# Performance work log

Hardware: AMD Instinct MI355X
Metric: run time of the kernel (lower is better)

## Reference

```python
import jax, jax.numpy as jnp
import numpy as np
import math

NEG_INF = -1e9
ALPHA = 1.0


def setup_inputs() -> dict:
    key = jax.random.key(0)
    B, T, S, C = 32, 1024, 512, 384
    k1, k2 = jax.random.split(key)
    epsilon = jax.random.normal(k1, (B, T, C), dtype=jnp.float32)
    conditional_inputs = jax.random.normal(k2, (B, S, C), dtype=jnp.float32)
    targets_lengths = jnp.full((B,), T, dtype=jnp.int32)
    condition_lengths = jnp.full((B,), S, dtype=jnp.int32)
    return {
        "epsilon": epsilon,
        "conditional_inputs": conditional_inputs,
        "targets_lengths": targets_lengths,
        "condition_lengths": condition_lengths,
    }


def _forward_dp(E):
    """Log-partition forward DP. E = alpha*Wr, [B,T,S].
    mu[t,j] = E[t,j] + logaddexp(mu[t-1,j], mu[t-1,j-1]); path starts at (0,0)."""
    B, T, S = E.shape
    start = jnp.where(jnp.arange(S) == 0, 0.0, NEG_INF)
    init = E[:, 0, :] + start[None, :]

    def step(mu_prev, e_t):
        shifted = jnp.concatenate([jnp.full((B, 1), NEG_INF, mu_prev.dtype), mu_prev[:, :-1]], axis=1)
        mu_t = e_t + jnp.logaddexp(mu_prev, shifted)
        return mu_t, mu_t

    _, mus = jax.lax.scan(step, init, jnp.moveaxis(E[:, 1:], 1, 0))
    return jnp.concatenate([init[:, None], jnp.moveaxis(mus, 0, 1)], axis=1)  # [B,T,S]


def _backward_dp(E):
    """Backward messages. beta[T-1,j] = 0 at j=S-1 else -inf;
    beta[t,j] = logaddexp(beta[t+1,j]+E[t+1,j], beta[t+1,j+1]+E[t+1,j+1])."""
    B, T, S = E.shape
    init = jnp.broadcast_to(jnp.where(jnp.arange(S) == S - 1, 0.0, NEG_INF), (B, S))

    def step(b_next, e_next):
        m = b_next + e_next
        shifted = jnp.concatenate([m[:, 1:], jnp.full((B, 1), NEG_INF, m.dtype)], axis=1)
        b_t = jnp.logaddexp(m, shifted)
        return b_t, b_t

    _, bs = jax.lax.scan(step, init, jnp.moveaxis(E[:, 1:], 1, 0), reverse=True)
    return jnp.concatenate([jnp.moveaxis(bs, 0, 1), init[:, None]], axis=1)  # [B,T,S]


def _maximum_path(logpi):
    """Viterbi over monotonic paths (stay at j or step to j from j-1 each t).
    Returns binary path [B,T,S]."""
    B, T, S = logpi.shape
    start = jnp.where(jnp.arange(S) == 0, 0.0, NEG_INF)
    init = logpi[:, 0, :] + start[None, :]

    def step(v_prev, lp_t):
        shifted = jnp.concatenate([jnp.full((B, 1), NEG_INF, v_prev.dtype), v_prev[:, :-1]], axis=1)
        v_t = lp_t + jnp.maximum(v_prev, shifted)
        move = shifted > v_prev  # True => predecessor is j-1
        return v_t, move

    _, moves = jax.lax.scan(step, init, jnp.moveaxis(logpi[:, 1:], 1, 0))  # [T-1,B,S]

    j_last = jnp.full((B,), S - 1, dtype=jnp.int32)

    def back(j, move_t):
        came = jnp.take_along_axis(move_t, j[:, None].astype(jnp.int32), axis=1)[:, 0]
        j_prev = j - came.astype(jnp.int32)
        return j_prev, j

    j0, js = jax.lax.scan(back, j_last, moves, reverse=True)  # js[i] = j at time i+1
    js_all = jnp.concatenate([j0[None], js], axis=0)  # [T,B]
    return jax.nn.one_hot(jnp.moveaxis(js_all, 0, 1), S, dtype=logpi.dtype)  # [B,T,S]


def reference(epsilon, conditional_inputs, targets_lengths, condition_lengths):
    B, T, C = epsilon.shape
    S = conditional_inputs.shape[1]
    # initial gaussian sample log-prob, masked by target lengths
    logp_eps = -0.5 * (epsilon ** 2 + math.log(2.0 * math.pi))
    tmask = (jnp.arange(T)[None, :] < targets_lengths[:, None]).astype(epsilon.dtype)
    logprobs = jnp.sum(tmask[:, :, None] * logp_eps, axis=(1, 2))

    z = epsilon  # Glow is external; treated as identity flow (logdet = 0)

    # score matrix + softmax over the target axis (dim 1), as in the source
    Wr = jnp.einsum("btc,bsc->bts", z, conditional_inputs)
    Wr = jax.nn.softmax(Wr, axis=1)

    E = ALPHA * Wr
    mu = _forward_dp(E)
    mu_N = mu[:, -1, -1]
    beta = _backward_dp(E)
    logpi = mu + beta - mu_N[:, None, None]  # posterior node log-marginals

    path = _maximum_path(logpi)  # [B,T,S] binary alignment
    sample_logprob = ALPHA * jnp.sum(path * Wr, axis=(1, 2)) - mu_N
    logprobs = logprobs + sample_logprob
    return path, logprobs
```

## Files before the change

### kernel.cpp

```cpp
#include <hip/hip_runtime.h>
#include <cstdint>
#include <cstddef>

#define B_ 32
#define T_ 1024
#define S_ 512
#define C_ 384
#define HALF_LOG_2PI 0.91893853320467274178f
#define LN2F 0.69314718055994530942f
#define INV_LN2F 1.44269504088896340736f

typedef unsigned short u16;
typedef unsigned long long u64;
typedef __attribute__((ext_vector_type(8))) short bf16x8;
typedef __attribute__((ext_vector_type(4))) float f32x4;

__device__ __forceinline__ unsigned rne16(float f) {
    unsigned b = __float_as_uint(f);
    return (b + 0x7FFFu + ((b >> 16) & 1u)) >> 16;
}
__device__ __forceinline__ uint4 pack8f(float a0, float a1, float a2, float a3,
                                        float a4, float a5, float a6, float a7) {
    uint4 q;
    q.x = rne16(a0) | (rne16(a1) << 16);
    q.y = rne16(a2) | (rne16(a3) << 16);
    q.z = rne16(a4) | (rne16(a5) << 16);
    q.w = rne16(a6) | (rne16(a7) << 16);
    return q;
}
#define UNPK(q, p)                                                              \
    float p##0 = __uint_as_float((q).x << 16),                                  \
          p##1 = __uint_as_float((q).x & 0xFFFF0000u),                          \
          p##2 = __uint_as_float((q).y << 16),                                  \
          p##3 = __uint_as_float((q).y & 0xFFFF0000u),                          \
          p##4 = __uint_as_float((q).z << 16),                                  \
          p##5 = __uint_as_float((q).z & 0xFFFF0000u),                          \
          p##6 = __uint_as_float((q).w << 16),                                  \
          p##7 = __uint_as_float((q).w & 0xFFFF0000u)

#define PROW(t) (*(const uint4*)(Pb  + (size_t)(t) * S_ + l8))
#define BROW(t) (*(const uint4*)(Btb + (size_t)(t) * S_ + l8))

template <int CTRL>
__device__ __forceinline__ float fdpp0(float x) {
    return __uint_as_float((unsigned)__builtin_amdgcn_update_dpp(
        0, (int)__float_as_uint(x), CTRL, 0xF, 0xF, true));
}
__device__ __forceinline__ float wave_fmax(float x) {
    x = fmaxf(x, fdpp0<0x121>(x));
    x = fmaxf(x, fdpp0<0x122>(x));
    x = fmaxf(x, fdpp0<0x124>(x));
    x = fmaxf(x, fdpp0<0x128>(x));
    float a = __uint_as_float((unsigned)__builtin_amdgcn_readlane((int)__float_as_uint(x), 0));
    float b = __uint_as_float((unsigned)__builtin_amdgcn_readlane((int)__float_as_uint(x), 16));
    float c = __uint_as_float((unsigned)__builtin_amdgcn_readlane((int)__float_as_uint(x), 32));
    float d = __uint_as_float((unsigned)__builtin_amdgcn_readlane((int)__float_as_uint(x), 48));
    return fmaxf(fmaxf(a, b), fmaxf(c, d));
}

__device__ __forceinline__ void gll16(const u16* g, u16* l) {
    __builtin_amdgcn_global_load_lds(
        (const __attribute__((address_space(1))) void*)g,
        (__attribute__((address_space(3))) void*)l, 16, 0, 0);
}
#define WAITV(N) do { asm volatile("s_waitcnt vmcnt(" #N ")" ::: "memory");     \
                      __builtin_amdgcn_sched_barrier(0); } while (0)
#define FENCE_LGKM() do { asm volatile("s_waitcnt lgkmcnt(0)" ::: "memory");    \
                          __builtin_amdgcn_sched_barrier(0); } while (0)

__global__ __launch_bounds__(256) void k_pre(const float* __restrict__ eps,
                                             const float* __restrict__ cond,
                                             const int* __restrict__ tlen,
                                             float* __restrict__ lp_part,
                                             u16* __restrict__ Abf,
                                             u16* __restrict__ Bbf) {
    if (blockIdx.x < 1536) {
        const int b = blockIdx.x / 48, chunk = blockIdx.x % 48;
        const int len = tlen[b];
        const float* base = eps + (size_t)b * T_ * C_ + (size_t)chunk * 8192;
        u16* obase = Abf + (size_t)b * T_ * C_ + (size_t)chunk * 8192;
        float acc = 0.f;
        for (int g = threadIdx.x; g < 1024; g += 256) {
            float4 v0 = *(const float4*)(base + g * 8);
            float4 v1 = *(const float4*)(base + g * 8 + 4);
            int t = (chunk * 8192 + g * 8) / C_;
            if (t < len)
                acc += v0.x*v0.x + v0.y*v0.y + v0.z*v0.z + v0.w*v0.w
                     + v1.x*v1.x + v1.y*v1.y + v1.z*v1.z + v1.w*v1.w;
            *(uint4*)(obase + g * 8) = pack8f(v0.x, v0.y, v0.z, v0.w,
                                              v1.x, v1.y, v1.z, v1.w);
        }
        __shared__ float red[256];
        red[threadIdx.x] = acc;
        __syncthreads();
        for (int o = 128; o > 0; o >>= 1) {
            if (threadIdx.x < o) red[threadIdx.x] += red[threadIdx.x + o];
            __syncthreads();
        }
        if (threadIdx.x == 0) lp_part[blockIdx.x] = -0.5f * red[0];
    } else {
        const size_t n8 = (size_t)B_ * S_ * C_ / 8;
        for (size_t i = (size_t)(blockIdx.x - 1536) * 256 + threadIdx.x; i < n8;
             i += (size_t)512 * 256) {
            float4 v0 = *(const float4*)(cond + i * 8);
            float4 v1 = *(const float4*)(cond + i * 8 + 4);
            *(uint4*)(Bbf + i * 8) = pack8f(v0.x, v0.y, v0.z, v0.w,
                                            v1.x, v1.y, v1.z, v1.w);
        }
    }
}

__global__ __launch_bounds__(256) void k_gemm(const u16* __restrict__ A,
                                              const u16* __restrict__ Bc,
                                              u16* __restrict__ Wb) {
    __shared__ u16 Al[4096];
    __shared__ u16 Bl[4096];
    const int wgid = blockIdx.x;
    const int xcd  = wgid & 7;
    const int rest = wgid >> 3;
    const int b    = (rest >> 5) * 8 + xcd;
    const int tile = rest & 31;
    const int m0 = (tile >> 2) * 128;
    const int n0 = (tile & 3) * 128;
    const int tid = threadIdx.x;
    const int lane = tid & 63, wid = tid >> 6;
    const int wy = wid >> 1, wx = wid & 1;
    const int r15 = lane & 15, kg = lane >> 4;
    const u16* Ab = A  + (size_t)b * T_ * C_;
    const u16* Bb = Bc + (size_t)b * S_ * C_;

    f32x4 acc[4][4];
#pragma unroll
    for (int i = 0; i < 4; ++i)
#pragma unroll
        for (int j = 0; j < 4; ++j) acc[i][j] = (f32x4){0.f, 0.f, 0.f, 0.f};

    const int row0 = tid >> 2, o0 = tid & 3;
    const int row1 = row0 + 64;
    const int wb0 = (row0 * 64 + o0 * 16) ^ (((row0 >> 1) & 7) << 4);
    const int wb1 = (row1 * 64 + o0 * 16) ^ (((row1 >> 1) & 7) << 4);
    const int rswz = ((r15 >> 1) & 7) << 4;

    for (int k0 = 0; k0 < C_; k0 += 32) {
        uint4 a0 = *(const uint4*)(Ab + (size_t)(m0 + row0) * C_ + k0 + o0 * 8);
        uint4 a1 = *(const uint4*)(Ab + (size_t)(m0 + row1) * C_ + k0 + o0 * 8);
        uint4 c0 = *(const uint4*)(Bb + (size_t)(n0 + row0) * C_ + k0 + o0 * 8);
        uint4 c1 = *(const uint4*)(Bb + (size_t)(n0 + row1) * C_ + k0 + o0 * 8);
        __syncthreads();
        *(uint4*)((char*)Al + wb0) = a0;
        *(uint4*)((char*)Al + wb1) = a1;
        *(uint4*)((char*)Bl + wb0) = c0;
        *(uint4*)((char*)Bl + wb1) = c1;
        __syncthreads();
        bf16x8 af[4], bfb[4];
#pragma unroll
        for (int ar = 0; ar < 4; ++ar) {
            int row = wy * 64 + ar * 16 + r15;
            af[ar] = *(const bf16x8*)((const char*)Al + ((row * 64 + kg * 16) ^ rswz));
        }
#pragma unroll
        for (int bc = 0; bc < 4; ++bc) {
            int row = wx * 64 + bc * 16 + r15;
            bfb[bc] = *(const bf16x8*)((const char*)Bl + ((row * 64 + kg * 16) ^ rswz));
        }
#pragma unroll
        for (int ar = 0; ar < 4; ++ar)
#pragma unroll
            for (int bc = 0; bc < 4; ++bc)
                acc[ar][bc] = __builtin_amdgcn_mfma_f32_16x16x32_bf16(
                    af[ar], bfb[bc], acc[ar][bc], 0, 0, 0);
    }
#pragma unroll
    for (int ar = 0; ar < 4; ++ar) {
        int t = m0 + wy * 64 + ar * 16 + kg * 4;
#pragma unroll
        for (int bc = 0; bc < 4; ++bc) {
            int s = n0 + wx * 64 + bc * 16 + r15;
            u16* dst = Wb + ((size_t)b * T_ + t) * S_ + s;
#pragma unroll
            for (int r = 0; r < 4; ++r) dst[(size_t)r * S_] = (u16)rne16(acc[ar][bc][r]);
        }
    }
}

#define COLU(i, xa, xb, xc, xd) do {                                            \
    float nm = fmaxf(fmaxf(fmaxf(m[i], xa), xb), fmaxf(xc, xd));                \
    s[i] = s[i] * __builtin_amdgcn_exp2f((m[i] - nm) * INV_LN2F)                \
         + __builtin_amdgcn_exp2f((xa - nm) * INV_LN2F)                         \
         + __builtin_amdgcn_exp2f((xb - nm) * INV_LN2F)                         \
         + __builtin_amdgcn_exp2f((xc - nm) * INV_LN2F)                         \
         + __builtin_amdgcn_exp2f((xd - nm) * INV_LN2F);                        \
    m[i] = nm;                                                                  \
} while (0)

__global__ __launch_bounds__(256) void k_stats1(const u16* __restrict__ Wb,
                                                float* __restrict__ pmax,
                                                float* __restrict__ psum) {
    __shared__ float smax[4][S_];
    __shared__ float ssum[4][S_];
    const int c = blockIdx.x & 3;
    const int b = blockIdx.x >> 2;
    const int w = threadIdx.x >> 6, l = threadIdx.x & 63;
    const u16* base = Wb + (size_t)b * T_ * S_ + (size_t)(c * 256 + w * 64) * S_ + l * 8;
    float m[8], s[8];
#pragma unroll
    for (int i = 0; i < 8; ++i) { m[i] = -3.0e38f; s[i] = 0.f; }
    for (int t = 0; t < 64; t += 4) {
        uint4 q0 = *(const uint4*)(base + (size_t)(t + 0) * S_);
        uint4 q1 = *(const uint4*)(base + (size_t)(t + 1) * S_);
        uint4 q2 = *(const uint4*)(base + (size_t)(t + 2) * S_);
        uint4 q3 = *(const uint4*)(base + (size_t)(t + 3) * S_);
        UNPK(q0, xa); UNPK(q1, xb); UNPK(q2, xc); UNPK(q3, xd);
        COLU(0, xa0, xb0, xc0, xd0);
        COLU(1, xa1, xb1, xc1, xd1);
        COLU(2, xa2, xb2, xc2, xd2);
        COLU(3, xa3, xb3, xc3, xd3);
        COLU(4, xa4, xb4, xc4, xd4);
        COLU(5, xa5, xb5, xc5, xd5);
        COLU(6, xa6, xb6, xc6, xd6);
        COLU(7, xa7, xb7, xc7, xd7);
    }
#pragma unroll
    for (int i = 0; i < 8; ++i) {
        smax[w][l * 8 + i] = m[i];
        ssum[w][l * 8 + i] = s[i];
    }
    __syncthreads();
    for (int col = threadIdx.x; col < S_; col += 256) {
        float m0 = smax[0][col], m1 = smax[1][col];
        float m2 = smax[2][col], m3 = smax[3][col];
        float nm = fmaxf(fmaxf(m0, m1), fmaxf(m2, m3));
        float ss = ssum[0][col] * __builtin_amdgcn_exp2f((m0 - nm) * INV_LN2F)
                 + ssum[1][col] * __builtin_amdgcn_exp2f((m1 - nm) * INV_LN2F)
                 + ssum[2][col] * __builtin_amdgcn_exp2f((m2 - nm) * INV_LN2F)
                 + ssum[3][col] * __builtin_amdgcn_exp2f((m3 - nm) * INV_LN2F);
        pmax[(size_t)c * B_ * S_ + b * S_ + col] = nm;
        psum[(size_t)c * B_ * S_ + b * S_ + col] = ss;
    }
}

__global__ __launch_bounds__(256) void k_stats2(const float* __restrict__ pmax,
                                                const float* __restrict__ psum,
                                                float* __restrict__ cmax,
                                                float* __restrict__ cinv) {
    const int i = blockIdx.x * 256 + threadIdx.x;
    float m0 = pmax[i], m1 = pmax[(size_t)B_ * S_ + i];
    float m2 = pmax[(size_t)2 * B_ * S_ + i], m3 = pmax[(size_t)3 * B_ * S_ + i];
    float m = fmaxf(fmaxf(m0, m1), fmaxf(m2, m3));
    float s = psum[i] * expf(m0 - m)
            + psum[(size_t)B_ * S_ + i] * expf(m1 - m)
            + psum[(size_t)2 * B_ * S_ + i] * expf(m2 - m)
            + psum[(size_t)3 * B_ * S_ + i] * expf(m3 - m);
    cmax[i] = m;
    cinv[i] = 1.0f / s;
}

__global__ __launch_bounds__(256) void k_pack(const u16* __restrict__ Wb,
                                              const float* __restrict__ cmax,
                                              const float* __restrict__ cinv,
                                              u16* __restrict__ P) {
    const size_t total8 = (size_t)B_ * T_ * S_ / 8;
    for (size_t i = (size_t)blockIdx.x * 256 + threadIdx.x; i < total8;
         i += (size_t)gridDim.x * 256) {
        size_t base = i * 8;
        int s = (int)(base & (S_ - 1));
        int b = (int)(base >> 19);
        uint4 xq = *(const uint4*)(Wb + base);
        UNPK(xq, x);
        float4 mA = *(const float4*)(cmax + (size_t)b * S_ + s);
        float4 mB = *(const float4*)(cmax + (size_t)b * S_ + s + 4);
        float4 iA = *(const float4*)(cinv + (size_t)b * S_ + s);
        float4 iB = *(const float4*)(cinv + (size_t)b * S_ + s + 4);
        float w0 = __builtin_amdgcn_exp2f(fmaf(x0, INV_LN2F, -mA.x * INV_LN2F)) * iA.x;
        float w1 = __builtin_amdgcn_exp2f(fmaf(x1, INV_LN2F, -mA.y * INV_LN2F)) * iA.y;
        float w2 = __builtin_amdgcn_exp2f(fmaf(x2, INV_LN2F, -mA.z * INV_LN2F)) * iA.z;
        float w3 = __builtin_amdgcn_exp2f(fmaf(x3, INV_LN2F, -mA.w * INV_LN2F)) * iA.w;
        float w4 = __builtin_amdgcn_exp2f(fmaf(x4, INV_LN2F, -mB.x * INV_LN2F)) * iB.x;
        float w5 = __builtin_amdgcn_exp2f(fmaf(x5, INV_LN2F, -mB.y * INV_LN2F)) * iB.y;
        float w6 = __builtin_amdgcn_exp2f(fmaf(x6, INV_LN2F, -mB.z * INV_LN2F)) * iB.z;
        float w7 = __builtin_amdgcn_exp2f(fmaf(x7, INV_LN2F, -mB.w * INV_LN2F)) * iB.w;
        float p0 = __builtin_amdgcn_exp2f(fmaf(w0, INV_LN2F, -2.0f));
        float p1 = __builtin_amdgcn_exp2f(fmaf(w1, INV_LN2F, -2.0f));
        float p2 = __builtin_amdgcn_exp2f(fmaf(w2, INV_LN2F, -2.0f));
        float p3 = __builtin_amdgcn_exp2f(fmaf(w3, INV_LN2F, -2.0f));
        float p4 = __builtin_amdgcn_exp2f(fmaf(w4, INV_LN2F, -2.0f));
        float p5 = __builtin_amdgcn_exp2f(fmaf(w5, INV_LN2F, -2.0f));
        float p6 = __builtin_amdgcn_exp2f(fmaf(w6, INV_LN2F, -2.0f));
        float p7 = __builtin_amdgcn_exp2f(fmaf(w7, INV_LN2F, -2.0f));
        *(uint4*)(P + base) = pack8f(p0, p1, p2, p3, p4, p5, p6, p7);
    }
}

#define RENORM_B() do {                                                         \
    float mx_ = wave_fmax(fmaxf(fmaxf(fmaxf(m0,m1),fmaxf(m2,m3)),               \
                                fmaxf(fmaxf(m4,m5),fmaxf(m6,m7))));             \
    int eb_ = (__float_as_int(mx_) >> 23) & 255;                                \
    float sc_ = (eb_ > 0) ? __int_as_float((254 - eb_) << 23) : 1.0f;           \
    m0*=sc_; m1*=sc_; m2*=sc_; m3*=sc_; m4*=sc_; m5*=sc_; m6*=sc_; m7*=sc_;     \
} while (0)

#define BSTEPD(tt, jj) do {                                                     \
    uint4 q_ = *(const uint4*)&Pl[buf][jj][l8];                                 \
    UNPK(q_, eP);                                                               \
    float z0=m0*eP0, z1=m1*eP1, z2=m2*eP2, z3=m3*eP3;                           \
    float z4=m4*eP4, z5=m5*eP5, z6=m6*eP6, z7=m7*eP7;                           \
    float rt = fdpp0<0x130>(z0);                \
    m0=z0+z1; m1=z1+z2; m2=z2+z3; m3=z3+z4;                                     \
    m4=z4+z5; m5=z5+z6; m6=z6+z7; m7=z7+rt;                                     \
    if ((tt) < w0 + 32) {                                                       \
        uint4 st;                                                               \
        asm("v_cvt_pk_bf16_f32 %0, %1, %2" : "=v"(st.x) : "v"(m0), "v"(m1));    \
        asm("v_cvt_pk_bf16_f32 %0, %1, %2" : "=v"(st.y) : "v"(m2), "v"(m3));    \
        asm("v_cvt_pk_bf16_f32 %0, %1, %2" : "=v"(st.z) : "v"(m4), "v"(m5));    \
        asm("v_cvt_pk_bf16_f32 %0, %1, %2" : "=v"(st.w) : "v"(m6), "v"(m7));    \
        *(uint4*)(Bb + (size_t)(tt) * S_ + l8) = st;                            \
    }                                                                           \
} while (0)

__global__ __launch_bounds__(64) void k_beta(const u16* __restrict__ P,
                                             u16* __restrict__ Bt) {
    __shared__ u16 Pl[2][8][S_];
    const int l = threadIdx.x, l8 = l * 8;
    const int xcd = blockIdx.x & 7;
    const int idx = blockIdx.x >> 3;
    const int c = idx & 31;
    const int b = ((idx >> 5) << 3) + xcd;
    const int w0 = c * 32;
    const u16* Pb = P  + (size_t)b * T_ * S_;
    u16*      Bb = Bt + (size_t)b * T_ * S_;
    float m0, m1, m2, m3, m4, m5, m6, m7;
    int te = w0 + 63;
    if (te > 1023) te = 1023;
    if (te == 1023) {
        m0 = m1 = m2 = m3 = m4 = m5 = m6 = 0.f;
        m7 = (l == 63) ? 1.f : 0.f;
        if (1023 < w0 + 32) {
            uint4 st;
            asm("v_cvt_pk_bf16_f32 %0, %1, %2" : "=v"(st.x) : "v"(m0), "v"(m1));
            asm("v_cvt_pk_bf16_f32 %0, %1, %2" : "=v"(st.y) : "v"(m2), "v"(m3));
            asm("v_cvt_pk_bf16_f32 %0, %1, %2" : "=v"(st.z) : "v"(m4), "v"(m5));
            asm("v_cvt_pk_bf16_f32 %0, %1, %2" : "=v"(st.w) : "v"(m6), "v"(m7));
            *(uint4*)(Bb + (size_t)1023 * S_ + l8) = st;
        }
    } else {
        m0 = m1 = m2 = m3 = m4 = m5 = m6 = m7 = 1.f;
    }
    const int cnt = te - w0;
    const int ng = (cnt + 1) >> 3;
#pragma unroll
    for (int r = 0; r < 8; ++r)
        gll16(Pb + (size_t)(te - r) * S_ + l8, &Pl[0][r][0]);
#pragma unroll
    for (int r = 0; r < 8; ++r)
        gll16(Pb + (size_t)(te - 8 - r) * S_ + l8, &Pl[1][r][0]);
    int tt = te - 1;
    int buf = 0;
    for (int g = 0; g < ng - 1; ++g) {
        WAITV(8);
        BSTEPD(tt - 0, 0);  BSTEPD(tt - 1, 1);  BSTEPD(tt - 2, 2);  BSTEPD(tt - 3, 3);
        BSTEPD(tt - 4, 4);  BSTEPD(tt - 5, 5);  BSTEPD(tt - 6, 6);  BSTEPD(tt - 7, 7);
        RENORM_B();
        FENCE_LGKM();
        if (g + 2 < ng) {
            const int bs = te - 8 * (g + 2);
#pragma unroll
            for (int r = 0; r < 8; ++r)
                gll16(Pb + (size_t)(bs - r) * S_ + l8, &Pl[buf][r][0]);
        }
        __builtin_amdgcn_sched_barrier(0);
        buf ^= 1;
        tt -= 8;
    }
    WAITV(0);
    BSTEPD(tt - 0, 0);  BSTEPD(tt - 1, 1);  BSTEPD(tt - 2, 2);  BSTEPD(tt - 3, 3);
    BSTEPD(tt - 4, 4);  BSTEPD(tt - 5, 5);  BSTEPD(tt - 6, 6);
}

#define RENORM_MI() do {                                                        \
    float mx_ = wave_fmax(fmaxf(fmaxf(fmaxf(m0,m1),fmaxf(m2,m3)),               \
                                fmaxf(fmaxf(m4,m5),fmaxf(m6,m7))));             \
    int eb_ = (__float_as_int(mx_) >> 23) & 255;                                \
    float sc_ = (eb_ > 0) ? __int_as_float((254 - eb_) << 23) : 1.0f;           \
    if (eb_ > 0) ioffM += eb_ - 127;                                            \
    m0*=sc_; m1*=sc_; m2*=sc_; m3*=sc_; m4*=sc_; m5*=sc_; m6*=sc_; m7*=sc_;     \
} while (0)

#define RENORM_VR() do {                                                        \
    float mx_ = wave_fmax(fmaxf(fmaxf(fmaxf(v0,v1),fmaxf(v2,v3)),               \
                                fmaxf(fmaxf(v4,v5),fmaxf(v6,v7))));             \
    int eb_ = (__float_as_int(mx_) >> 23) & 255;                                \
    float sc_ = (eb_ > 0) ? __int_as_float((254 - eb_) << 23) : 0.0f;           \
    float ad_ = (eb_ > 0) ? 0.f : 1.f;                                          \
    v0=fmaf(v0,sc_,ad_); v1=fmaf(v1,sc_,ad_); v2=fmaf(v2,sc_,ad_);              \
    v3=fmaf(v3,sc_,ad_); v4=fmaf(v4,sc_,ad_); v5=fmaf(v5,sc_,ad_);              \
    v6=fmaf(v6,sc_,ad_); v7=fmaf(v7,sc_,ad_);                                   \
} while (0)

#define VSTEPD(TT, jj) do {                                                     \
    uint4 qp_ = *(const uint4*)&Pl[buf][jj][l8];                                \
    uint4 qb_ = *(const uint4*)&Bl[buf][jj][l8];                                \
    UNPK(qp_, eP); UNPK(qb_, eB);                                               \
    float lf = fdpp0<0x138>(m7);                 \
    float n0 = eP0*(m0+lf), n1 = eP1*(m1+m0);                                   \
    float n2 = eP2*(m2+m1), n3 = eP3*(m3+m2);                                   \
    float n4 = eP4*(m4+m3), n5 = eP5*(m5+m4);                                   \
    float n6 = eP6*(m6+m5), n7 = eP7*(m7+m6);                                   \
    float vlf = fdpp0<0x138>(v7);                                               \
    if ((TT) >= w0) {                                                           \
        unsigned cc0=(vlf>v0)?1u:0u, cc1=(v0>v1)?2u:0u, cc2=(v1>v2)?4u:0u,      \
                 cc3=(v2>v3)?8u:0u,  cc4=(v3>v4)?16u:0u, cc5=(v4>v5)?32u:0u,    \
                 cc6=(v5>v6)?64u:0u, cc7=(v6>v7)?128u:0u;                       \
        acc |= ((u64)(cc0|cc1|cc2|cc3|cc4|cc5|cc6|cc7)) << (((TT)&7)*8);        \
        if (((TT)&7) == 7) { mrow[((TT)>>3)*64 + l] = acc; acc = 0ULL; }        \
    }                                                                           \
    float w0v=(n0*eB0)*fmaxf(v0,vlf), w1v=(n1*eB1)*fmaxf(v1,v0);                \
    float w2v=(n2*eB2)*fmaxf(v2,v1),  w3v=(n3*eB3)*fmaxf(v3,v2);                \
    float w4v=(n4*eB4)*fmaxf(v4,v3),  w5v=(n5*eB5)*fmaxf(v5,v4);                \
    float w6v=(n6*eB6)*fmaxf(v6,v5),  w7v=(n7*eB7)*fmaxf(v7,v6);                \
    m0=n0;m1=n1;m2=n2;m3=n3;m4=n4;m5=n5;m6=n6;m7=n7;                            \
    v0=w0v;v1=w1v;v2=w2v;v3=w3v;v4=w4v;v5=w5v;v6=w6v;v7=w7v;                    \
    if ((TT) == wexp) { wex = __shfl(m0, 2 * c); wio = ioffM; }                 \
} while (0)

__global__ __launch_bounds__(64) void k_vit(const u16* __restrict__ P,
                                            const u16* __restrict__ Bt,
                                            u64* __restrict__ mbg,
                                            float* __restrict__ elog,
                                            float* __restrict__ wlg) {
    __shared__ u16 Pl[2][8][S_];
    __shared__ u16 Bl[2][8][S_];
    const int l = threadIdx.x, l8 = l * 8;
    const int xcd = blockIdx.x & 7;
    const int idx = blockIdx.x >> 3;
    const int c = idx & 31;
    const int b = ((idx >> 5) << 3) + xcd;
    const int w0 = c * 32, tend = w0 + 31;
    const int t0 = (w0 >= 32) ? (w0 - 32) : 0;
    const int wexp = w0 - 1;
    const u16* Pb  = P  + (size_t)b * T_ * S_;
    const u16* Btb = Bt + (size_t)b * T_ * S_;
    u64* mrow = mbg + (size_t)b * 8192;

    float m0,m1,m2,m3,m4,m5,m6,m7, v0,v1,v2,v3,v4,v5,v6,v7;
    int ioffM = 0;
    float wex = 1.f; int wio = 0;
    {
        uint4 qp = PROW(t0); UNPK(qp, eP);
        uint4 qb = BROW(t0); UNPK(qb, eB);
        if (t0 == 0) {
            m0 = (l == 0) ? eP0 : 0.f;
            m1 = 0.f; m2 = 0.f; m3 = 0.f; m4 = 0.f; m5 = 0.f; m6 = 0.f; m7 = 0.f;
        } else {
            m0 = eP0; m1 = eP1; m2 = eP2; m3 = eP3;
            m4 = eP4; m5 = eP5; m6 = eP6; m7 = eP7;
        }
        v0 = m0*eB0; v1 = m1*eB1; v2 = m2*eB2; v3 = m3*eB3;
        v4 = m4*eB4; v5 = m5*eB5; v6 = m6*eB6; v7 = m7*eB7;
    }
    u64 acc = 0ULL;
    const int cnt = tend - t0;
    const int ng = (cnt + 1) >> 3;
#pragma unroll
    for (int r = 0; r < 8; ++r) {
        gll16(Pb  + (size_t)(t0 + 1 + r) * S_ + l8, &Pl[0][r][0]);
        gll16(Btb + (size_t)(t0 + 1 + r) * S_ + l8, &Bl[0][r][0]);
    }
#pragma unroll
    for (int r = 0; r < 8; ++r) {
        gll16(Pb  + (size_t)(t0 + 9 + r) * S_ + l8, &Pl[1][r][0]);
        gll16(Btb + (size_t)(t0 + 9 + r) * S_ + l8, &Bl[1][r][0]);
    }
    int t = t0 + 1;
    int buf = 0;
    for (int g = 0; g < ng - 1; ++g) {
        WAITV(16);
        VSTEPD(t + 0, 0);  VSTEPD(t + 1, 1);  VSTEPD(t + 2, 2);  VSTEPD(t + 3, 3);
        VSTEPD(t + 4, 4);  VSTEPD(t + 5, 5);  VSTEPD(t + 6, 6);  VSTEPD(t + 7, 7);
        RENORM_MI();
        RENORM_VR();
        FENCE_LGKM();
        if (g + 2 < ng) {
            const int bs = t0 + 1 + 8 * (g + 2);
#pragma unroll
            for (int r = 0; r < 8; ++r) {
                gll16(Pb  + (size_t)(bs + r) * S_ + l8, &Pl[buf][r][0]);
                gll16(Btb + (size_t)(bs + r) * S_ + l8, &Bl[buf][r][0]);
            }
        }
        __builtin_amdgcn_sched_barrier(0);
        buf ^= 1;
        t += 8;
    }
    WAITV(0);
    VSTEPD(t + 0, 0);  VSTEPD(t + 1, 1);  VSTEPD(t + 2, 2);  VSTEPD(t + 3, 3);
    VSTEPD(t + 4, 4);  VSTEPD(t + 5, 5);  VSTEPD(t + 6, 6);

    float eex = (c == 31) ? __shfl(m7, 63) : __shfl(m0, 2 * (c + 1));
    if (l == 0) {
        elog[b * 32 + c] = __builtin_amdgcn_logf(fmaxf(eex, 1e-35f)) + (float)ioffM;
        if (c >= 1)
            wlg[b * 32 + c] = __builtin_amdgcn_logf(fmaxf(wex, 1e-35f)) + (float)wio;
    }
}

__global__ __launch_bounds__(512) void k_map(const u64* __restrict__ mbg,
                                             u16* __restrict__ map) {
    __shared__ u64 mb[4][64];
    const int b = blockIdx.x >> 5, c = blockIdx.x & 31;
    const int tid = threadIdx.x;
    const u64* src = mbg + (size_t)b * 8192 + (size_t)(4 * c) * 64;
    if (tid < 128) ((uint4*)&mb[0][0])[tid] = ((const uint4*)src)[tid];
    __syncthreads();
    int jj = tid;
    const int kmin = (c == 0) ? 1 : 0;
    for (int k = 31; k >= kmin; --k) {
        u64 word = mb[k >> 3][jj >> 3];
        jj -= (int)((word >> ((k & 7) * 8 + (jj & 7))) & 1ULL);
    }
    map[((size_t)b * 32 + c) * 512 + tid] = (u16)jj;
}

__global__ __launch_bounds__(256) void k_btr2(const u64* __restrict__ mbg,
                                              const u16* __restrict__ map,
                                              int* __restrict__ js) {
    __shared__ u64 mb[128][64];
    __shared__ u16 cent[32];
    const int b = blockIdx.x, tid = threadIdx.x;
    const uint4* src = (const uint4*)(mbg + (size_t)b * 8192);
    uint4* dst = (uint4*)&mb[0][0];
    for (int i = tid; i < 4096; i += 256) dst[i] = src[i];
    if (tid == 0) {
        int jj = 511;
        cent[31] = 511;
        for (int c = 31; c >= 1; --c) {
            jj = (int)map[((size_t)b * 32 + c) * 512 + jj];
            cent[c - 1] = (u16)jj;
        }
    }
    __syncthreads();
    if (tid < 32) {
        const int c = tid;
        int jj = (int)cent[c];
        js[b * T_ + 32 * c + 31] = jj;
        const int kmin = (c == 0) ? 1 : 0;
        for (int k = 31; k >= kmin; --k) {
            const int t = 32 * c + k;
            u64 word = mb[t >> 3][jj >> 3];
            jj -= (int)((word >> ((t & 7) * 8 + (jj & 7))) & 1ULL);
            js[b * T_ + t - 1] = jj;
        }
    }
}

__global__ __launch_bounds__(256) void k_out(const int* __restrict__ js,
                                             const u16* __restrict__ P,
                                             const float* __restrict__ lp_part,
                                             const int* __restrict__ tlen,
                                             const float* __restrict__ elog,
                                             const float* __restrict__ wlg,
                                             float* __restrict__ outp,
                                             float* __restrict__ out_lp) {
    if (blockIdx.x < 4096) {
        const size_t total4 = (size_t)B_ * T_ * S_ / 4;
        float4* O = (float4*)outp;
        for (size_t i = (size_t)blockIdx.x * 256 + threadIdx.x; i < total4;
             i += (size_t)4096 * 256) {
            size_t base = i * 4;
            int s = (int)(base & (S_ - 1));
            int row = (int)(base >> 9);
            int jt = js[row];
            float4 o;
            o.x = (s == jt) ? 1.f : 0.f;
            o.y = (s + 1 == jt) ? 1.f : 0.f;
            o.z = (s + 2 == jt) ? 1.f : 0.f;
            o.w = (s + 3 == jt) ? 1.f : 0.f;
            O[i] = o;
        }
    } else {
        const int b = blockIdx.x - 4096;
        float acc = 0.f;
        for (int t = threadIdx.x; t < T_; t += 256) {
            int jt = js[b * T_ + t];
            unsigned u = P[((size_t)b * T_ + t) * S_ + jt];
            acc += __builtin_amdgcn_logf(__uint_as_float(u << 16));
        }
        __shared__ float red[256];
        red[threadIdx.x] = acc;
        __syncthreads();
        for (int o = 128; o > 0; o >>= 1) {
            if (threadIdx.x < o) red[threadIdx.x] += red[threadIdx.x + o];
            __syncthreads();
        }
        if (threadIdx.x == 0) {
            float basep = 0.f;
            for (int i = 0; i < 48; ++i) basep += lp_part[b * 48 + i];
            float mu2n = elog[b * 32 + 31];
            for (int cc = 1; cc < 32; ++cc)
                mu2n += elog[b * 32 + cc - 1] - wlg[b * 32 + cc];
            out_lp[b] = basep - HALF_LOG_2PI * ((float)tlen[b] * C_)
                        + LN2F * (red[0] - mu2n);
        }
    }
}

extern "C" void kernel_launch(void* const* d_in, const int* in_sizes, int n_in,
                              void* d_out, int out_size, void* d_ws, size_t ws_size,
                              hipStream_t stream) {
    const float* eps  = (const float*)d_in[0];
    const float* cond = (const float*)d_in[1];
    const int* tlen   = (const int*)d_in[2];

    float* out_path = (float*)d_out;
    float* out_lp   = out_path + (size_t)B_ * T_ * S_;

    const size_t NBTS = (size_t)B_ * T_ * S_;
    char* w = (char*)d_ws;
    u16*   Wb   = (u16*)w;
    u16*   P    = Wb + NBTS;
    u16*   Bt   = P + NBTS;
    u16*   Abf  = Bt + NBTS;
    u16*   Bbf  = Abf + (size_t)B_ * T_ * C_;
    u64*   mbg  = (u64*)(Bbf + (size_t)B_ * S_ * C_);
    float* pmax = (float*)(mbg + (size_t)B_ * 8192);
    float* psum = pmax + (size_t)4 * B_ * S_;
    float* cmax = psum + (size_t)4 * B_ * S_;
    float* cinv = cmax + (size_t)B_ * S_;
    float* lp_part = cinv + (size_t)B_ * S_;
    float* elog = lp_part + B_ * 48;
    float* wlg  = elog + B_ * 32;
    int*   js   = (int*)(wlg + B_ * 32);
    u16*   map  = (u16*)(js + B_ * T_);

    k_pre<<<2048, 256, 0, stream>>>(eps, cond, tlen, lp_part, Abf, Bbf);
    k_gemm<<<1024, 256, 0, stream>>>(Abf, Bbf, Wb);
    k_stats1<<<B_ * 4, 256, 0, stream>>>(Wb, pmax, psum);
    k_stats2<<<B_ * S_ / 256, 256, 0, stream>>>(pmax, psum, cmax, cinv);
    k_pack<<<2048, 256, 0, stream>>>(Wb, cmax, cinv, P);
    k_beta<<<B_ * 32, 64, 0, stream>>>(P, Bt);
    k_vit<<<B_ * 32, 64, 0, stream>>>(P, Bt, mbg, elog, wlg);
    k_map<<<B_ * 32, 512, 0, stream>>>(mbg, map);
    k_btr2<<<B_, 256, 0, stream>>>(mbg, map, js);
    k_out<<<4096 + B_, 256, 0, stream>>>(js, P, lp_part, tlen, elog, wlg,
                                         out_path, out_lp);
}
```

Before: 154.5 us.

## Fuse softmax column stats into GEMM epilogue and drop the P pack pass

The GEMM epilogue now computes per-column partial max and sum-exp over its 64-row slab and reduces them across lanes with shuffles, which removes the separate k_stats1 pass that re-read the whole score matrix. The k_pack kernel that materialised the softmax-exponentiated matrix P is also removed. k_beta, k_vit and k_out instead recompute the two exp2 calls per element from the raw bf16 scores plus the column max and inverse sum. This saves two full passes over a 32x1024x512 bf16 array, in exchange for extra transcendental work inside the latency-bound DP kernels and 16 partial slabs for k_stats2 to combine instead of 4.

```diff
diff --git a/kernel.cpp b/kernel.cpp
--- a/kernel.cpp
+++ b/kernel.cpp
@@ -38,7 +38,12 @@
           p##6 = __uint_as_float((q).w << 16),                                  \
           p##7 = __uint_as_float((q).w & 0xFFFF0000u)
 
-#define PROW(t) (*(const uint4*)(Pb  + (size_t)(t) * S_ + l8))
+#define P1(x, km, ki)                                                           \
+    __builtin_amdgcn_exp2f(fmaf(                                                \
+        __builtin_amdgcn_exp2f(fmaf((x), INV_LN2F, -(km))) * (ki),              \
+        INV_LN2F, -2.0f))
+
+#define WROW(t) (*(const uint4*)(Wbb + (size_t)(t) * S_ + l8))
 #define BROW(t) (*(const uint4*)(Btb + (size_t)(t) * S_ + l8))
 
 template <int CTRL>
@@ -112,7 +117,9 @@
 
 __global__ __launch_bounds__(256) void k_gemm(const u16* __restrict__ A,
                                               const u16* __restrict__ Bc,
-                                              u16* __restrict__ Wb) {
+                                              u16* __restrict__ Wb,
+                                              float* __restrict__ pmax,
+                                              float* __restrict__ psum) {
     __shared__ u16 Al[4096];
     __shared__ u16 Bl[4096];
     const int wgid = blockIdx.x;
@@ -181,61 +188,43 @@
             for (int r = 0; r < 4; ++r) dst[(size_t)r * S_] = (u16)rne16(acc[ar][bc][r]);
         }
     }
-}
-
-#define COLU(i, xa, xb, xc, xd) do {                                            \
-    float nm = fmaxf(fmaxf(fmaxf(m[i], xa), xb), fmaxf(xc, xd));                \
-    s[i] = s[i] * __builtin_amdgcn_exp2f((m[i] - nm) * INV_LN2F)                \
-         + __builtin_amdgcn_exp2f((xa - nm) * INV_LN2F)                         \
-         + __builtin_amdgcn_exp2f((xb - nm) * INV_LN2F)                         \
-         + __builtin_amdgcn_exp2f((xc - nm) * INV_LN2F)                         \
-         + __builtin_amdgcn_exp2f((xd - nm) * INV_LN2F);                        \
-    m[i] = nm;                                                                  \
-} while (0)
-
-__global__ __launch_bounds__(256) void k_stats1(const u16* __restrict__ Wb,
-                                                float* __restrict__ pmax,
-                                                float* __restrict__ psum) {
-    __shared__ float smax[4][S_];
-    __shared__ float ssum[4][S_];
-    const int c = blockIdx.x & 3;
-    const int b = blockIdx.x >> 2;
-    const int w = threadIdx.x >> 6, l = threadIdx.x & 63;
-    const u16* base = Wb + (size_t)b * T_ * S_ + (size_t)(c * 256 + w * 64) * S_ + l * 8;
-    float m[8], s[8];
-#pragma unroll
-    for (int i = 0; i < 8; ++i) { m[i] = -3.0e38f; s[i] = 0.f; }
-    for (int t = 0; t < 64; t += 4) {
-        uint4 q0 = *(const uint4*)(base + (size_t)(t + 0) * S_);
-        uint4 q1 = *(const uint4*)(base + (size_t)(t + 1) * S_);
-        uint4 q2 = *(const uint4*)(base + (size_t)(t + 2) * S_);
-        uint4 q3 = *(const uint4*)(base + (size_t)(t + 3) * S_);
-        UNPK(q0, xa); UNPK(q1, xb); UNPK(q2, xc); UNPK(q3, xd);
-        COLU(0, xa0, xb0, xc0, xd0);
-        COLU(1, xa1, xb1, xc1, xd1);
-        COLU(2, xa2, xb2, xc2, xd2);
-        COLU(3, xa3, xb3, xc3, xd3);
-        COLU(4, xa4, xb4, xc4, xd4);
-        COLU(5, xa5, xb5, xc5, xd5);
-        COLU(6, xa6, xb6, xc6, xd6);
-        COLU(7, xa7, xb7, xc7, xd7);
-    }
-#pragma unroll
-    for (int i = 0; i < 8; ++i) {
-        smax[w][l * 8 + i] = m[i];
-        ssum[w][l * 8 + i] = s[i];
-    }
-    __syncthreads();
-    for (int col = threadIdx.x; col < S_; col += 256) {
-        float m0 = smax[0][col], m1 = smax[1][col];
-        float m2 = smax[2][col], m3 = smax[3][col];
-        float nm = fmaxf(fmaxf(m0, m1), fmaxf(m2, m3));
-        float ss = ssum[0][col] * __builtin_amdgcn_exp2f((m0 - nm) * INV_LN2F)
-                 + ssum[1][col] * __builtin_amdgcn_exp2f((m1 - nm) * INV_LN2F)
-                 + ssum[2][col] * __builtin_amdgcn_exp2f((m2 - nm) * INV_LN2F)
-                 + ssum[3][col] * __builtin_amdgcn_exp2f((m3 - nm) * INV_LN2F);
-        pmax[(size_t)c * B_ * S_ + b * S_ + col] = nm;
-        psum[(size_t)c * B_ * S_ + b * S_ + col] = ss;
+    float pm[4], ps[4];
+#pragma unroll
+    for (int bc = 0; bc < 4; ++bc) {
+        float mx = -3.0e38f;
+#pragma unroll
+        for (int ar = 0; ar < 4; ++ar)
+#pragma unroll
+            for (int r = 0; r < 4; ++r) mx = fmaxf(mx, acc[ar][bc][r]);
+        float s = 0.f;
+#pragma unroll
+        for (int ar = 0; ar < 4; ++ar)
+#pragma unroll
+            for (int r = 0; r < 4; ++r)
+                s += __builtin_amdgcn_exp2f((acc[ar][bc][r] - mx) * INV_LN2F);
+        pm[bc] = mx; ps[bc] = s;
+    }
+#pragma unroll
+    for (int bc = 0; bc < 4; ++bc) {
+        float m2 = __shfl_xor(pm[bc], 16), s2 = __shfl_xor(ps[bc], 16);
+        float nm = fmaxf(pm[bc], m2);
+        ps[bc] = ps[bc] * __builtin_amdgcn_exp2f((pm[bc] - nm) * INV_LN2F)
+               + s2     * __builtin_amdgcn_exp2f((m2     - nm) * INV_LN2F);
+        pm[bc] = nm;
+        m2 = __shfl_xor(pm[bc], 32); s2 = __shfl_xor(ps[bc], 32);
+        nm = fmaxf(pm[bc], m2);
+        ps[bc] = ps[bc] * __builtin_amdgcn_exp2f((pm[bc] - nm) * INV_LN2F)
+               + s2     * __builtin_amdgcn_exp2f((m2     - nm) * INV_LN2F);
+        pm[bc] = nm;
+    }
+    if (kg == 0) {
+        const int tc = (m0 >> 6) + wy;
+#pragma unroll
+        for (int bc = 0; bc < 4; ++bc) {
+            int col = n0 + wx * 64 + bc * 16 + r15;
+            pmax[((size_t)tc * B_ + b) * S_ + col] = pm[bc];
+            psum[((size_t)tc * B_ + b) * S_ + col] = ps[bc];
+        }
     }
 }
 
@@ -243,52 +232,16 @@
                                                 const float* __restrict__ psum,
                                                 float* __restrict__ cmax,
                                                 float* __restrict__ cinv) {
-    const int i = blockIdx.x * 256 + threadIdx.x;
-    float m0 = pmax[i], m1 = pmax[(size_t)B_ * S_ + i];
-    float m2 = pmax[(size_t)2 * B_ * S_ + i], m3 = pmax[(size_t)3 * B_ * S_ + i];
-    float m = fmaxf(fmaxf(m0, m1), fmaxf(m2, m3));
-    float s = psum[i] * expf(m0 - m)
-            + psum[(size_t)B_ * S_ + i] * expf(m1 - m)
-            + psum[(size_t)2 * B_ * S_ + i] * expf(m2 - m)
-            + psum[(size_t)3 * B_ * S_ + i] * expf(m3 - m);
+    const size_t i = (size_t)blockIdx.x * 256 + threadIdx.x;
+    const size_t BS = (size_t)B_ * S_;
+    float m = -3.0e38f;
+    for (int cc = 0; cc < 16; ++cc) m = fmaxf(m, pmax[cc * BS + i]);
+    float s = 0.f;
+    for (int cc = 0; cc < 16; ++cc)
+        s += psum[cc * BS + i] *
+             __builtin_amdgcn_exp2f((pmax[cc * BS + i] - m) * INV_LN2F);
     cmax[i] = m;
     cinv[i] = 1.0f / s;
-}
-
-__global__ __launch_bounds__(256) void k_pack(const u16* __restrict__ Wb,
-                                              const float* __restrict__ cmax,
-                                              const float* __restrict__ cinv,
-                                              u16* __restrict__ P) {
-    const size_t total8 = (size_t)B_ * T_ * S_ / 8;
-    for (size_t i = (size_t)blockIdx.x * 256 + threadIdx.x; i < total8;
-         i += (size_t)gridDim.x * 256) {
-        size_t base = i * 8;
-        int s = (int)(base & (S_ - 1));
-        int b = (int)(base >> 19);
-        uint4 xq = *(const uint4*)(Wb + base);
-        UNPK(xq, x);
-        float4 mA = *(const float4*)(cmax + (size_t)b * S_ + s);
-        float4 mB = *(const float4*)(cmax + (size_t)b * S_ + s + 4);
-        float4 iA = *(const float4*)(cinv + (size_t)b * S_ + s);
-        float4 iB = *(const float4*)(cinv + (size_t)b * S_ + s + 4);
-        float w0 = __builtin_amdgcn_exp2f(fmaf(x0, INV_LN2F, -mA.x * INV_LN2F)) * iA.x;
-        float w1 = __builtin_amdgcn_exp2f(fmaf(x1, INV_LN2F, -mA.y * INV_LN2F)) * iA.y;
-        float w2 = __builtin_amdgcn_exp2f(fmaf(x2, INV_LN2F, -mA.z * INV_LN2F)) * iA.z;
-        float w3 = __builtin_amdgcn_exp2f(fmaf(x3, INV_LN2F, -mA.w * INV_LN2F)) * iA.w;
-        float w4 = __builtin_amdgcn_exp2f(fmaf(x4, INV_LN2F, -mB.x * INV_LN2F)) * iB.x;
-        float w5 = __builtin_amdgcn_exp2f(fmaf(x5, INV_LN2F, -mB.y * INV_LN2F)) * iB.y;
-        float w6 = __builtin_amdgcn_exp2f(fmaf(x6, INV_LN2F, -mB.z * INV_LN2F)) * iB.z;
-        float w7 = __builtin_amdgcn_exp2f(fmaf(x7, INV_LN2F, -mB.w * INV_LN2F)) * iB.w;
-        float p0 = __builtin_amdgcn_exp2f(fmaf(w0, INV_LN2F, -2.0f));
-        float p1 = __builtin_amdgcn_exp2f(fmaf(w1, INV_LN2F, -2.0f));
-        float p2 = __builtin_amdgcn_exp2f(fmaf(w2, INV_LN2F, -2.0f));
-        float p3 = __builtin_amdgcn_exp2f(fmaf(w3, INV_LN2F, -2.0f));
-        float p4 = __builtin_amdgcn_exp2f(fmaf(w4, INV_LN2F, -2.0f));
-        float p5 = __builtin_amdgcn_exp2f(fmaf(w5, INV_LN2F, -2.0f));
-        float p6 = __builtin_amdgcn_exp2f(fmaf(w6, INV_LN2F, -2.0f));
-        float p7 = __builtin_amdgcn_exp2f(fmaf(w7, INV_LN2F, -2.0f));
-        *(uint4*)(P + base) = pack8f(p0, p1, p2, p3, p4, p5, p6, p7);
-    }
 }
 
 #define RENORM_B() do {                                                         \
@@ -301,7 +254,11 @@
 
 #define BSTEPD(tt, jj) do {                                                     \
     uint4 q_ = *(const uint4*)&Pl[buf][jj][l8];                                 \
-    UNPK(q_, eP);                                                               \
+    UNPK(q_, xr);                                                               \
+    float eP0=P1(xr0,km0,ki0), eP1=P1(xr1,km1,ki1);                             \
+    float eP2=P1(xr2,km2,ki2), eP3=P1(xr3,km3,ki3);                             \
+    float eP4=P1(xr4,km4,ki4), eP5=P1(xr5,km5,ki5);                             \
+    float eP6=P1(xr6,km6,ki6), eP7=P1(xr7,km7,ki7);                             \
     float z0=m0*eP0, z1=m1*eP1, z2=m2*eP2, z3=m3*eP3;                           \
     float z4=m4*eP4, z5=m5*eP5, z6=m6*eP6, z7=m7*eP7;                           \
     float rt = fdpp0<0x130>(z0);                \
@@ -317,7 +274,9 @@
     }                                                                           \
 } while (0)
 
-__global__ __launch_bounds__(64) void k_beta(const u16* __restrict__ P,
+__global__ __launch_bounds__(64) void k_beta(const u16* __restrict__ Wb,
+                                             const float* __restrict__ cmax,
+                                             const float* __restrict__ cinv,
                                              u16* __restrict__ Bt) {
     __shared__ u16 Pl[2][8][S_];
     const int l = threadIdx.x, l8 = l * 8;
@@ -326,8 +285,17 @@
     const int c = idx & 31;
     const int b = ((idx >> 5) << 3) + xcd;
     const int w0 = c * 32;
-    const u16* Pb = P  + (size_t)b * T_ * S_;
+    const u16* Pb = Wb + (size_t)b * T_ * S_;
     u16*      Bb = Bt + (size_t)b * T_ * S_;
+    const float4 cA = *(const float4*)(cmax + (size_t)b * S_ + l8);
+    const float4 cB = *(const float4*)(cmax + (size_t)b * S_ + l8 + 4);
+    const float4 iA = *(const float4*)(cinv + (size_t)b * S_ + l8);
+    const float4 iB = *(const float4*)(cinv + (size_t)b * S_ + l8 + 4);
+    const float km0=cA.x*INV_LN2F, km1=cA.y*INV_LN2F, km2=cA.z*INV_LN2F, km3=cA.w*INV_LN2F;
+    const float km4=cB.x*INV_LN2F, km5=cB.y*INV_LN2F, km6=cB.z*INV_LN2F, km7=cB.w*INV_LN2F;
+    const float ki0=iA.x, ki1=iA.y, ki2=iA.z, ki3=iA.w;
+    const float ki4=iB.x, ki5=iB.y, ki6=iB.z, ki7=iB.w;
+
     float m0, m1, m2, m3, m4, m5, m6, m7;
     int te = w0 + 63;
     if (te > 1023) te = 1023;
@@ -399,7 +367,11 @@
 #define VSTEPD(TT, jj) do {                                                     \
     uint4 qp_ = *(const uint4*)&Pl[buf][jj][l8];                                \
     uint4 qb_ = *(const uint4*)&Bl[buf][jj][l8];                                \
-    UNPK(qp_, eP); UNPK(qb_, eB);                                               \
+    UNPK(qp_, xr); UNPK(qb_, eB);                                               \
+    float eP0=P1(xr0,km0,ki0), eP1=P1(xr1,km1,ki1);                             \
+    float eP2=P1(xr2,km2,ki2), eP3=P1(xr3,km3,ki3);                             \
+    float eP4=P1(xr4,km4,ki4), eP5=P1(xr5,km5,ki5);                             \
+    float eP6=P1(xr6,km6,ki6), eP7=P1(xr7,km7,ki7);                             \
     float lf = fdpp0<0x138>(m7);                 \
     float n0 = eP0*(m0+lf), n1 = eP1*(m1+m0);                                   \
     float n2 = eP2*(m2+m1), n3 = eP3*(m3+m2);                                   \
@@ -422,8 +394,10 @@
     if ((TT) == wexp) { wex = __shfl(m0, 2 * c); wio = ioffM; }                 \
 } while (0)
 
-__global__ __launch_bounds__(64) void k_vit(const u16* __restrict__ P,
+__global__ __launch_bounds__(64) void k_vit(const u16* __restrict__ Wb,
                                             const u16* __restrict__ Bt,
+                                            const float* __restrict__ cmax,
+                                            const float* __restrict__ cinv,
                                             u64* __restrict__ mbg,
                                             float* __restrict__ elog,
                                             float* __restrict__ wlg) {
@@ -437,22 +411,35 @@
     const int w0 = c * 32, tend = w0 + 31;
     const int t0 = (w0 >= 32) ? (w0 - 32) : 0;
     const int wexp = w0 - 1;
-    const u16* Pb  = P  + (size_t)b * T_ * S_;
+    const u16* Wbb = Wb + (size_t)b * T_ * S_;
+    const u16* Pb  = Wbb;
     const u16* Btb = Bt + (size_t)b * T_ * S_;
     u64* mrow = mbg + (size_t)b * 8192;
+    const float4 cA = *(const float4*)(cmax + (size_t)b * S_ + l8);
+    const float4 cB = *(const float4*)(cmax + (size_t)b * S_ + l8 + 4);
+    const float4 iA = *(const float4*)(cinv + (size_t)b * S_ + l8);
+    const float4 iB = *(const float4*)(cinv + (size_t)b * S_ + l8 + 4);
+    const float km0=cA.x*INV_LN2F, km1=cA.y*INV_LN2F, km2=cA.z*INV_LN2F, km3=cA.w*INV_LN2F;
+    const float km4=cB.x*INV_LN2F, km5=cB.y*INV_LN2F, km6=cB.z*INV_LN2F, km7=cB.w*INV_LN2F;
+    const float ki0=iA.x, ki1=iA.y, ki2=iA.z, ki3=iA.w;
+    const float ki4=iB.x, ki5=iB.y, ki6=iB.z, ki7=iB.w;
 
     float m0,m1,m2,m3,m4,m5,m6,m7, v0,v1,v2,v3,v4,v5,v6,v7;
     int ioffM = 0;
     float wex = 1.f; int wio = 0;
     {
-        uint4 qp = PROW(t0); UNPK(qp, eP);
+        uint4 qp = WROW(t0); UNPK(qp, xr);
         uint4 qb = BROW(t0); UNPK(qb, eB);
+        float p0i=P1(xr0,km0,ki0), p1i=P1(xr1,km1,ki1);
+        float p2i=P1(xr2,km2,ki2), p3i=P1(xr3,km3,ki3);
+        float p4i=P1(xr4,km4,ki4), p5i=P1(xr5,km5,ki5);
+        float p6i=P1(xr6,km6,ki6), p7i=P1(xr7,km7,ki7);
         if (t0 == 0) {
-            m0 = (l == 0) ? eP0 : 0.f;
+            m0 = (l == 0) ? p0i : 0.f;
             m1 = 0.f; m2 = 0.f; m3 = 0.f; m4 = 0.f; m5 = 0.f; m6 = 0.f; m7 = 0.f;
         } else {
-            m0 = eP0; m1 = eP1; m2 = eP2; m3 = eP3;
-            m4 = eP4; m5 = eP5; m6 = eP6; m7 = eP7;
+            m0 = p0i; m1 = p1i; m2 = p2i; m3 = p3i;
+            m4 = p4i; m5 = p5i; m6 = p6i; m7 = p7i;
         }
         v0 = m0*eB0; v1 = m1*eB1; v2 = m2*eB2; v3 = m3*eB3;
         v4 = m4*eB4; v5 = m5*eB5; v6 = m6*eB6; v7 = m7*eB7;
@@ -553,7 +540,9 @@
 }
 
 __global__ __launch_bounds__(256) void k_out(const int* __restrict__ js,
-                                             const u16* __restrict__ P,
+                                             const u16* __restrict__ Wb,
+                                             const float* __restrict__ cmax,
+                                             const float* __restrict__ cinv,
                                              const float* __restrict__ lp_part,
                                              const int* __restrict__ tlen,
                                              const float* __restrict__ elog,
@@ -581,8 +570,12 @@
         float acc = 0.f;
         for (int t = threadIdx.x; t < T_; t += 256) {
             int jt = js[b * T_ + t];
-            unsigned u = P[((size_t)b * T_ + t) * S_ + jt];
-            acc += __builtin_amdgcn_logf(__uint_as_float(u << 16));
+            float x = __uint_as_float(
+                (unsigned)Wb[((size_t)b * T_ + t) * S_ + jt] << 16);
+            float cm = cmax[(size_t)b * S_ + jt];
+            float ci = cinv[(size_t)b * S_ + jt];
+            float w = __builtin_amdgcn_exp2f(fmaf(x, INV_LN2F, -cm * INV_LN2F)) * ci;
+            acc += fmaf(w, INV_LN2F, -2.0f);
         }
         __shared__ float red[256];
         red[threadIdx.x] = acc;
@@ -616,14 +609,13 @@
     const size_t NBTS = (size_t)B_ * T_ * S_;
     char* w = (char*)d_ws;
     u16*   Wb   = (u16*)w;
-    u16*   P    = Wb + NBTS;
-    u16*   Bt   = P + NBTS;
+    u16*   Bt   = Wb + NBTS;
     u16*   Abf  = Bt + NBTS;
     u16*   Bbf  = Abf + (size_t)B_ * T_ * C_;
     u64*   mbg  = (u64*)(Bbf + (size_t)B_ * S_ * C_);
     float* pmax = (float*)(mbg + (size_t)B_ * 8192);
-    float* psum = pmax + (size_t)4 * B_ * S_;
-    float* cmax = psum + (size_t)4 * B_ * S_;
+    float* psum = pmax + (size_t)16 * B_ * S_;
+    float* cmax = psum + (size_t)16 * B_ * S_;
     float* cinv = cmax + (size_t)B_ * S_;
     float* lp_part = cinv + (size_t)B_ * S_;
     float* elog = lp_part + B_ * 48;
@@ -632,14 +624,12 @@
     u16*   map  = (u16*)(js + B_ * T_);
 
     k_pre<<<2048, 256, 0, stream>>>(eps, cond, tlen, lp_part, Abf, Bbf);
-    k_gemm<<<1024, 256, 0, stream>>>(Abf, Bbf, Wb);
-    k_stats1<<<B_ * 4, 256, 0, stream>>>(Wb, pmax, psum);
+    k_gemm<<<1024, 256, 0, stream>>>(Abf, Bbf, Wb, pmax, psum);
     k_stats2<<<B_ * S_ / 256, 256, 0, stream>>>(pmax, psum, cmax, cinv);
-    k_pack<<<2048, 256, 0, stream>>>(Wb, cmax, cinv, P);
-    k_beta<<<B_ * 32, 64, 0, stream>>>(P, Bt);
-    k_vit<<<B_ * 32, 64, 0, stream>>>(P, Bt, mbg, elog, wlg);
+    k_beta<<<B_ * 32, 64, 0, stream>>>(Wb, cmax, cinv, Bt);
+    k_vit<<<B_ * 32, 64, 0, stream>>>(Wb, Bt, cmax, cinv, mbg, elog, wlg);
     k_map<<<B_ * 32, 512, 0, stream>>>(mbg, map);
     k_btr2<<<B_, 256, 0, stream>>>(mbg, map, js);
-    k_out<<<4096 + B_, 256, 0, stream>>>(js, P, lp_part, tlen, elog, wlg,
-                                         out_path, out_lp);
-}
+    k_out<<<4096 + B_, 256, 0, stream>>>(js, Wb, cmax, cinv, lp_part, tlen,
+                                         elog, wlg, out_path, out_lp);
+}
```

Result: faster. 148.1 us (median of 2 runs) (-4.1%).
